# Optimization experiments

Measured on AMD Instinct MI355X. Metric: run time of the kernel, lower is better.

Reference implementation:

```python
import math
import jax, jax.numpy as jnp
import numpy as np

N_HEAD = 32
N_KV_HEADS = 8
HEAD_DIM = 128
N_EMBD = 4096
B, T = 1, 2048


def apply_rope(x, cos, sin):
    # x: [B, H, T, D]; cos/sin: [T, D//2] -> broadcast over B, H
    half = x.shape[-1] // 2
    c = cos[None, None, :, :]
    s = sin[None, None, :, :]
    x1, x2 = x[..., :half], x[..., half:]
    return jnp.concatenate([x1 * c - x2 * s, x2 * c + x1 * s], axis=-1).astype(x.dtype)


def setup_inputs() -> dict:
    key = jax.random.key(0)
    ks = jax.random.split(key, 7)
    x = jax.random.normal(ks[0], (B, T, N_EMBD), dtype=jnp.float32)
    # realistic rope tables
    inv_freq = 1.0 / (10000.0 ** (jnp.arange(0, HEAD_DIM, 2, dtype=jnp.float32) / HEAD_DIM))
    angles = jnp.arange(T, dtype=jnp.float32)[:, None] * inv_freq[None, :]  # [T, D//2]
    rope_cos = jnp.cos(angles)
    rope_sin = jnp.sin(angles)
    sc = 1.0 / math.sqrt(N_EMBD)
    Wq = jax.random.normal(ks[1], (N_EMBD, N_HEAD * HEAD_DIM), dtype=jnp.float32) * sc
    Wk = jax.random.normal(ks[2], (N_EMBD, N_KV_HEADS * HEAD_DIM), dtype=jnp.float32) * sc
    Wv = jax.random.normal(ks[3], (N_EMBD, N_KV_HEADS * HEAD_DIM), dtype=jnp.float32) * sc
    Wo = jax.random.normal(ks[4], (N_HEAD * HEAD_DIM, N_EMBD), dtype=jnp.float32) * sc
    return {"x": x, "rope_cos": rope_cos, "rope_sin": rope_sin,
            "Wq": Wq, "Wk": Wk, "Wv": Wv, "Wo": Wo}


def reference(x, rope_cos, rope_sin, Wq, Wk, Wv, Wo):
    Bx, Tx, _ = x.shape
    n_rep = N_HEAD // N_KV_HEADS
    # QKV projections (no bias, Llama-style) -> [B, H, T, D]
    q = jnp.einsum('btd,df->btf', x, Wq).reshape(Bx, Tx, N_HEAD, HEAD_DIM).transpose(0, 2, 1, 3)
    k = jnp.einsum('btd,df->btf', x, Wk).reshape(Bx, Tx, N_KV_HEADS, HEAD_DIM).transpose(0, 2, 1, 3)
    v = jnp.einsum('btd,df->btf', x, Wv).reshape(Bx, Tx, N_KV_HEADS, HEAD_DIM).transpose(0, 2, 1, 3)
    q = apply_rope(q, rope_cos, rope_sin)
    k = apply_rope(k, rope_cos, rope_sin)
    # GQA: repeat_interleave kv heads to match query heads
    if n_rep > 1:
        k = jnp.repeat(k, n_rep, axis=1)
        v = jnp.repeat(v, n_rep, axis=1)
    scale = 1.0 / math.sqrt(HEAD_DIM)
    scores = jnp.einsum('bhqd,bhkd->bhqk', q, k) * scale  # [B, H, T, T]
    causal = jnp.tril(jnp.ones((Tx, Tx), dtype=bool))
    scores = jnp.where(causal[None, None, :, :], scores, jnp.finfo(scores.dtype).min)
    attn = jax.nn.softmax(scores, axis=-1)
    y = jnp.einsum('bhqk,bhkd->bhqd', attn, v)
    y = y.transpose(0, 2, 1, 3).reshape(Bx, Tx, N_HEAD * HEAD_DIM)
    return jnp.einsum('btf,fd->btd', y, Wo)
```

## Files before the change

kernel.cpp:

```cpp
#include <hip/hip_runtime.h>

typedef unsigned short u16;
typedef __bf16 bf16x8 __attribute__((ext_vector_type(8)));
typedef float f32x4 __attribute__((ext_vector_type(4)));

__device__ __forceinline__ u16 f2bf(float f) {
    unsigned int u = __builtin_bit_cast(unsigned int, f);
    u += 0x7fffu + ((u >> 16) & 1u);
    return (u16)(u >> 16);
}
__device__ __forceinline__ float bf2f(u16 b) {
    unsigned int u = ((unsigned int)b) << 16;
    return __builtin_bit_cast(float, u);
}
__device__ __forceinline__ void load_lds16(const void* g, void* l) {
    __builtin_amdgcn_global_load_lds((__attribute__((address_space(1))) void*)(g),
                                     (__attribute__((address_space(3))) void*)(l), 16, 0, 0);
}
__device__ __forceinline__ f32x4 mfma16(bf16x8 a, bf16x8 b, f32x4 c) {
    return __builtin_amdgcn_mfma_f32_16x16x32_bf16(a, b, c, 0, 0, 0);
}

__global__ __launch_bounds__(256) void k_cvt_bf16(const float* __restrict__ in,
                                                  u16* __restrict__ out, int n4) {
    int i = blockIdx.x * 256 + threadIdx.x;
    if (i < n4) {
        float4 v = ((const float4*)in)[i];
        unsigned int lo = (unsigned int)f2bf(v.x) | ((unsigned int)f2bf(v.y) << 16);
        unsigned int hi = (unsigned int)f2bf(v.z) | ((unsigned int)f2bf(v.w) << 16);
        ((uint2*)out)[i] = make_uint2(lo, hi);
    }
}

__global__ __launch_bounds__(256) void k_transpose_cvt(const float* __restrict__ W,
                                                       u16* __restrict__ Wt, int K, int N) {
    __shared__ u16 t[32][33];
    int tx = threadIdx.x & 31, ty = threadIdx.x >> 5;
    int n0 = blockIdx.x * 32, k0 = blockIdx.y * 32;
#pragma unroll
    for (int i = 0; i < 4; i++)
        t[ty + i * 8][tx] = f2bf(W[(size_t)(k0 + ty + i * 8) * N + n0 + tx]);
    __syncthreads();
#pragma unroll
    for (int i = 0; i < 4; i++)
        Wt[(size_t)(n0 + ty + i * 8) * K + k0 + tx] = t[tx][ty + i * 8];
}

__global__ __launch_bounds__(256) void k_transpose_v(const u16* __restrict__ QKV,
                                                     u16* __restrict__ Vt) {
    __shared__ u16 t[32][33];
    int tx = threadIdx.x & 31, ty = threadIdx.x >> 5;
    int t0 = blockIdx.x * 32, d0 = blockIdx.y * 32, kh = blockIdx.z;
#pragma unroll
    for (int i = 0; i < 4; i++)
        t[ty + i * 8][tx] = QKV[(size_t)(t0 + ty + i * 8) * 6144 + 5120 + kh * 128 + d0 + tx];
    __syncthreads();
#pragma unroll
    for (int i = 0; i < 4; i++)
        Vt[((size_t)kh * 128 + d0 + ty + i * 8) * 2048 + t0 + tx] = t[tx][ty + i * 8];
}

__global__ __launch_bounds__(256) void k_rope2(u16* __restrict__ QKV,
                                               const float* __restrict__ cosT,
                                               const float* __restrict__ sinT) {
    int idx = blockIdx.x * 256 + threadIdx.x;
    int d = idx & 63;
    int h = (idx >> 6) % 40;
    int tp = idx / (40 * 64);
    int col = h < 32 ? h * 128 : 4096 + (h - 32) * 128;
    size_t base = (size_t)tp * 6144 + col + d;
    float q1 = bf2f(QKV[base]), q2 = bf2f(QKV[base + 64]);
    float c = cosT[tp * 64 + d], s = sinT[tp * 64 + d];
    QKV[base] = f2bf(q1 * c - q2 * s);
    QKV[base + 64] = f2bf(q2 * c + q1 * s);
}

template <typename OutT>
__global__ __launch_bounds__(256) void k_gemm_bt(const u16* __restrict__ A,
                                                 const u16* __restrict__ B,
                                                 OutT* __restrict__ C, int M, int N, int K) {
    __shared__ u16 sA[128 * 32];
    __shared__ u16 sB[128 * 32];
    const int tid = threadIdx.x;
    const int wave = tid >> 6, lane = tid & 63;
    const int gx = (int)gridDim.x;
    const int nwg = gx * (int)gridDim.y;
    const int orig = (int)blockIdx.y * gx + (int)blockIdx.x;
    const int qq = nwg >> 3, rr8 = nwg & 7;
    const int xcd = orig & 7, bidx = orig >> 3;
    const int swz = (xcd < rr8 ? xcd * (qq + 1) : rr8 * (qq + 1) + (xcd - rr8) * qq) + bidx;
    const int m0 = (swz / gx) << 7;
    const int n0 = (swz % gx) << 7;
    const int wr = (wave >> 1) << 6, wc = (wave & 1) << 6;
    const int r0 = tid >> 2;
    const int kb = (tid & 3) << 4;
    const int fr = lane & 15;
    const int fkb = (lane >> 4) << 4;

    f32x4 acc[4][4] = {};
    const char* gA = (const char*)A + ((size_t)(m0 + r0) * K) * 2 + kb;
    const char* gB = (const char*)B + ((size_t)(n0 + r0) * K) * 2 + kb;
    char* lA = (char*)sA + wave * 1024;
    char* lB = (char*)sB + wave * 1024;
    const size_t rowskip = (size_t)64 * K * 2;

    for (int k0 = 0; k0 < K; k0 += 32) {
        load_lds16(gA, lA);
        load_lds16(gA + rowskip, lA + 4096);
        load_lds16(gB, lB);
        load_lds16(gB + rowskip, lB + 4096);
        gA += 64; gB += 64;
        __syncthreads();
        bf16x8 af[4], bg[4];
#pragma unroll
        for (int i = 0; i < 4; i++)
            af[i] = *(const bf16x8*)((const char*)sA + ((wr + i * 16 + fr) << 6) + fkb);
#pragma unroll
        for (int j = 0; j < 4; j++)
            bg[j] = *(const bf16x8*)((const char*)sB + ((wc + j * 16 + fr) << 6) + fkb);
#pragma unroll
        for (int i = 0; i < 4; i++)
#pragma unroll
            for (int j = 0; j < 4; j++)
                acc[i][j] = mfma16(af[i], bg[j], acc[i][j]);
        __syncthreads();
    }
    const int rr = (lane >> 4) << 2, cc = lane & 15;
#pragma unroll
    for (int i = 0; i < 4; i++)
#pragma unroll
        for (int j = 0; j < 4; j++)
#pragma unroll
            for (int r = 0; r < 4; r++) {
                float v = acc[i][j][r];
                OutT sv;
                if constexpr (sizeof(OutT) == 2) sv = f2bf(v); else sv = v;
                C[(size_t)(m0 + wr + i * 16 + rr + r) * N + (n0 + wc + j * 16 + cc)] = sv;
            }
}

__global__ __launch_bounds__(256, 2) void k_attn(const u16* __restrict__ Q,
                                                 const u16* __restrict__ K,
                                                 const u16* __restrict__ Vt,
                                                 u16* __restrict__ Y) {
    __shared__ u16 kt[64 * 128];
    __shared__ u16 vt[128 * 64];
    __shared__ u16 pl[4 * 16 * 64];
    const int tid = threadIdx.x;
    const int wave = tid >> 6, lane = tid & 63;
    const int l15 = lane & 15, l4 = lane >> 4;
    const int h = blockIdx.y, kh = h >> 2;
    const float scale = 0.08838834764831845f;

    char* ktb = (char*)kt;
    char* vtb = (char*)vt;
    char* plb = (char*)pl + wave * 2048;

#pragma unroll 1
    for (int qsel = 0; qsel < 2; qsel++) {
        const int qt = qsel == 0 ? blockIdx.x : 31 - blockIdx.x;
        const int qw = qt * 64 + wave * 16;

        bf16x8 aq[4];
#pragma unroll
        for (int kf = 0; kf < 4; kf++)
            aq[kf] = *(const bf16x8*)(Q + (size_t)(qw + l15) * 6144 + h * 128 + kf * 32 + l4 * 8);

        f32x4 o[8] = {};
        float mrow[4], lrow[4];
#pragma unroll
        for (int rg = 0; rg < 4; rg++) { mrow[rg] = -1e30f; lrow[rg] = 0.f; }

        const int nkt = qt + 1;
        for (int it = 0; it < nkt; ++it) {
            const int kbase = it << 6;
#pragma unroll
            for (int p = 0; p < 4; p++) {
                int ol = wave * 4096 + p * 1024 + lane * 16;
                int key = ol >> 8, db = ol & 255;
                int src = db ^ ((key & 7) << 4);
                load_lds16((const char*)K + ((size_t)(kbase + key) * 6144 + kh * 128) * 2 + src,
                           ktb + wave * 4096 + p * 1024);
            }
#pragma unroll
            for (int p = 0; p < 4; p++) {
                int ol = wave * 4096 + p * 1024 + lane * 16;
                int d = ol >> 7, kb2 = ol & 127;
                int src = kb2 ^ ((d & 7) << 4);
                load_lds16((const char*)Vt + ((size_t)(kh * 128 + d) * 2048 + kbase) * 2 + src,
                           vtb + wave * 4096 + p * 1024);
            }
            __syncthreads();

            f32x4 s[4];
#pragma unroll
            for (int tc = 0; tc < 4; tc++) {
                bf16x8 bk[4];
                const int key = tc * 16 + l15;
                const int swz = (key & 7) << 4;
#pragma unroll
                for (int kf = 0; kf < 4; kf++)
                    bk[kf] = *(const bf16x8*)(ktb + key * 256 + ((kf * 64 + l4 * 16) ^ swz));
                f32x4 sv = {0.f, 0.f, 0.f, 0.f};
#pragma unroll
                for (int kf = 0; kf < 4; kf++) sv = mfma16(aq[kf], bk[kf], sv);
                s[tc] = sv;
            }
#pragma unroll
            for (int rg = 0; rg < 4; rg++) {
                const int qrow = qw + l4 * 4 + rg;
                float mx = -1e30f;
#pragma unroll
                for (int tc = 0; tc < 4; tc++) {
                    float v = s[tc][rg] * scale;
                    int key = kbase + tc * 16 + l15;
                    v = (key > qrow) ? -1e30f : v;
                    s[tc][rg] = v;
                    mx = fmaxf(mx, v);
                }
                mx = fmaxf(mx, __shfl_xor(mx, 1));
                mx = fmaxf(mx, __shfl_xor(mx, 2));
                mx = fmaxf(mx, __shfl_xor(mx, 4));
                mx = fmaxf(mx, __shfl_xor(mx, 8));
                const float mold = mrow[rg];
                const float mnew = fmaxf(mold, mx);
                const float corr = __expf(mold - mnew);
                mrow[rg] = mnew;
                float rs = 0.f;
#pragma unroll
                for (int tc = 0; tc < 4; tc++) {
                    float p = __expf(s[tc][rg] - mnew);
                    s[tc][rg] = p;
                    rs += p;
                }
                rs += __shfl_xor(rs, 1);
                rs += __shfl_xor(rs, 2);
                rs += __shfl_xor(rs, 4);
                rs += __shfl_xor(rs, 8);
                lrow[rg] = lrow[rg] * corr + rs;
#pragma unroll
                for (int dc = 0; dc < 8; dc++) o[dc][rg] *= corr;
            }
#pragma unroll
            for (int rg = 0; rg < 4; rg++) {
                const int row = l4 * 4 + rg;
                const int swz = (row & 7) << 4;
#pragma unroll
                for (int tc = 0; tc < 4; tc++) {
                    const int cb = (tc * 16 + l15) * 2;
                    *(u16*)(plb + row * 128 + (cb ^ swz)) = f2bf(s[tc][rg]);
                }
            }
            bf16x8 pa[2];
            {
                const int row = l15;
                const int swz = (row & 7) << 4;
#pragma unroll
                for (int kf = 0; kf < 2; kf++)
                    pa[kf] = *(const bf16x8*)(plb + row * 128 + ((kf * 64 + l4 * 16) ^ swz));
            }
#pragma unroll
            for (int dc = 0; dc < 8; dc++) {
                bf16x8 vf[2];
                const int d = dc * 16 + l15;
                const int swz = (d & 7) << 4;
#pragma unroll
                for (int kf = 0; kf < 2; kf++)
                    vf[kf] = *(const bf16x8*)(vtb + d * 128 + ((kf * 64 + l4 * 16) ^ swz));
                o[dc] = mfma16(pa[0], vf[0], o[dc]);
                o[dc] = mfma16(pa[1], vf[1], o[dc]);
            }
            __syncthreads();
        }
#pragma unroll
        for (int rg = 0; rg < 4; rg++) {
            const float inv = 1.f / lrow[rg];
            const int row = qw + l4 * 4 + rg;
#pragma unroll
            for (int dc = 0; dc < 8; dc++)
                Y[(size_t)row * 4096 + h * 128 + dc * 16 + l15] = f2bf(o[dc][rg] * inv);
        }
        __syncthreads();
    }
}

extern "C" void kernel_launch(void* const* d_in, const int* in_sizes, int n_in,
                              void* d_out, int out_size, void* d_ws, size_t ws_size,
                              hipStream_t stream) {
    const float* x  = (const float*)d_in[0];
    const float* rc = (const float*)d_in[1];
    const float* rs = (const float*)d_in[2];
    const float* Wq = (const float*)d_in[3];
    const float* Wk = (const float*)d_in[4];
    const float* Wv = (const float*)d_in[5];
    const float* Wo = (const float*)d_in[6];
    float* out = (float*)d_out;

    char* ws = (char*)d_ws;
    u16* xb  = (u16*)(ws);
    u16* Wt  = (u16*)(ws + 16777216);
    u16* QKV = (u16*)(ws + 67108864);
    u16* Vtb = (u16*)(ws + 92274688);
    u16* Y   = xb;

    k_cvt_bf16<<<8192, 256, 0, stream>>>(x, xb, 2097152);
    k_transpose_cvt<<<dim3(128, 128), 256, 0, stream>>>(Wq, Wt, 4096, 4096);
    k_transpose_cvt<<<dim3(32, 128), 256, 0, stream>>>(Wk, Wt + (size_t)4096 * 4096, 4096, 1024);
    k_transpose_cvt<<<dim3(32, 128), 256, 0, stream>>>(Wv, Wt + (size_t)5120 * 4096, 4096, 1024);
    k_gemm_bt<u16><<<dim3(48, 16), 256, 0, stream>>>(xb, Wt, QKV, 2048, 6144, 4096);
    k_rope2<<<20480, 256, 0, stream>>>(QKV, rc, rs);
    k_transpose_v<<<dim3(64, 4, 8), 256, 0, stream>>>(QKV, Vtb);
    k_attn<<<dim3(16, 32), 256, 0, stream>>>(QKV, QKV + 4096, Vtb, Y);
    k_transpose_cvt<<<dim3(128, 128), 256, 0, stream>>>(Wo, Wt, 4096, 4096);
    k_gemm_bt<float><<<dim3(32, 16), 256, 0, stream>>>(Y, Wt, out, 2048, 4096, 4096);
}
```

Before: 570.4 us.

## Replace 128x128 GEMM with double-buffered 256x256 tile kernel using 512 threads

Both projection GEMMs now use a new kernel with 256x256 output tiles, 8 waves and 128KB of LDS. Global-to-LDS loads are double-buffered and split into two half-K stages synchronised with vmcnt waits. The LDS layout is swizzled to avoid bank conflicts, and s_setprio is raised around the MFMA bursts. The aim is more operand reuse per load and overlapping loads with compute, at the cost of far fewer workgroups (192 and 128), which leaves some CUs idle. Local variables in the attention kernel are renamed so they do not clash with the new macros.

```diff
diff --git a/kernel.cpp b/kernel.cpp
--- a/kernel.cpp
+++ b/kernel.cpp
@@ -75,67 +75,109 @@
     QKV[base + 64] = f2bf(q2 * c + q1 * s);
 }
 
+
+#define STAGE(G, base0, ldsOff, kt, kh)                                                     \
+    {                                                                                       \
+        _Pragma("unroll") for (int p = 0; p < 2; p++) {                                     \
+            int o = p * 8192 + o0;                                                          \
+            int row = o >> 6;                                                               \
+            int kb = (o & 48) ^ (((row >> 1) & 3) << 4);                                    \
+            load_lds16((const char*)(G) +                                                   \
+                           ((size_t)(base0 + row) * K + (kt) * 64 + (kh) * 32) * 2 + kb,    \
+                       lb + (ldsOff) + p * 8192 + waveB);                                   \
+        }                                                                                   \
+    }
+#define LDA(kh, bufv)                                                                       \
+    _Pragma("unroll") for (int fm = 0; fm < 8; fm++) {                                      \
+        int row = wmBase + fm * 16 + l15;                                                   \
+        af[fm] = *(const bf16x8*)(lb + (bufv) * 32768 + (kh) * 16384 + row * 64 +           \
+                                  ((l4 * 16) ^ (((row >> 1) & 3) << 4)));                   \
+    }
+#define LDB(fn, kh, bufv, dst)                                                              \
+    {                                                                                       \
+        int row = wnBase + (fn) * 16 + l15;                                                 \
+        dst = *(const bf16x8*)(lb + 65536 + (bufv) * 32768 + (kh) * 16384 + row * 64 +      \
+                               ((l4 * 16) ^ (((row >> 1) & 3) << 4)));                      \
+    }
+#define MFMA2(fnA, fnB)                                                                     \
+    __builtin_amdgcn_s_setprio(1);                                                          \
+    _Pragma("unroll") for (int fm = 0; fm < 8; fm++) {                                      \
+        acc[fm][fnA] = mfma16(af[fm], b0, acc[fm][fnA]);                                    \
+        acc[fm][fnB] = mfma16(af[fm], b1, acc[fm][fnB]);                                    \
+    }                                                                                       \
+    __builtin_amdgcn_s_setprio(0);
+
 template <typename OutT>
-__global__ __launch_bounds__(256) void k_gemm_bt(const u16* __restrict__ A,
-                                                 const u16* __restrict__ B,
-                                                 OutT* __restrict__ C, int M, int N, int K) {
-    __shared__ u16 sA[128 * 32];
-    __shared__ u16 sB[128 * 32];
+__global__ __launch_bounds__(512, 2) void k_gemm256(const u16* __restrict__ A,
+                                                    const u16* __restrict__ B,
+                                                    OutT* __restrict__ C, int M, int N, int K) {
+    __shared__ u16 lds[65536];
     const int tid = threadIdx.x;
-    const int wave = tid >> 6, lane = tid & 63;
+    const int lane = tid & 63, l15 = lane & 15, l4 = lane >> 4;
+    const int wave = tid >> 6;
+    const int wmBase = (wave >> 2) << 7;
+    const int wnBase = (wave & 3) << 6;
+    const int waveB = wave << 10;
+    const int o0 = tid * 16;
+
     const int gx = (int)gridDim.x;
     const int nwg = gx * (int)gridDim.y;
     const int orig = (int)blockIdx.y * gx + (int)blockIdx.x;
     const int qq = nwg >> 3, rr8 = nwg & 7;
     const int xcd = orig & 7, bidx = orig >> 3;
     const int swz = (xcd < rr8 ? xcd * (qq + 1) : rr8 * (qq + 1) + (xcd - rr8) * qq) + bidx;
-    const int m0 = (swz / gx) << 7;
-    const int n0 = (swz % gx) << 7;
-    const int wr = (wave >> 1) << 6, wc = (wave & 1) << 6;
-    const int r0 = tid >> 2;
-    const int kb = (tid & 3) << 4;
-    const int fr = lane & 15;
-    const int fkb = (lane >> 4) << 4;
-
-    f32x4 acc[4][4] = {};
-    const char* gA = (const char*)A + ((size_t)(m0 + r0) * K) * 2 + kb;
-    const char* gB = (const char*)B + ((size_t)(n0 + r0) * K) * 2 + kb;
-    char* lA = (char*)sA + wave * 1024;
-    char* lB = (char*)sB + wave * 1024;
-    const size_t rowskip = (size_t)64 * K * 2;
-
-    for (int k0 = 0; k0 < K; k0 += 32) {
-        load_lds16(gA, lA);
-        load_lds16(gA + rowskip, lA + 4096);
-        load_lds16(gB, lB);
-        load_lds16(gB + rowskip, lB + 4096);
-        gA += 64; gB += 64;
-        __syncthreads();
-        bf16x8 af[4], bg[4];
-#pragma unroll
-        for (int i = 0; i < 4; i++)
-            af[i] = *(const bf16x8*)((const char*)sA + ((wr + i * 16 + fr) << 6) + fkb);
-#pragma unroll
-        for (int j = 0; j < 4; j++)
-            bg[j] = *(const bf16x8*)((const char*)sB + ((wc + j * 16 + fr) << 6) + fkb);
-#pragma unroll
-        for (int i = 0; i < 4; i++)
-#pragma unroll
-            for (int j = 0; j < 4; j++)
-                acc[i][j] = mfma16(af[i], bg[j], acc[i][j]);
-        __syncthreads();
-    }
-    const int rr = (lane >> 4) << 2, cc = lane & 15;
-#pragma unroll
-    for (int i = 0; i < 4; i++)
-#pragma unroll
-        for (int j = 0; j < 4; j++)
+    const int m0 = (swz / gx) << 8;
+    const int n0 = (swz % gx) << 8;
+
+    char* lb = (char*)lds;
+    f32x4 acc[8][4] = {};
+    bf16x8 af[8], b0, b1;
+
+    STAGE(A, m0, 0, 0, 0);
+    STAGE(B, n0, 65536, 0, 0);
+    STAGE(A, m0, 16384, 0, 1);
+    STAGE(B, n0, 65536 + 16384, 0, 1);
+
+    const int NT = K >> 6;
+#pragma unroll 1
+    for (int t = 0; t < NT; ++t) {
+        const int buf = t & 1, nbuf = buf ^ 1;
+        const int nt = (t + 1 < NT) ? t + 1 : 0;
+        const int ab = nbuf * 32768, bb = 65536 + nbuf * 32768;
+        asm volatile("s_waitcnt vmcnt(4)" ::: "memory");
+        __builtin_amdgcn_s_barrier();
+        LDA(0, buf);
+        LDB(0, 0, buf, b0);
+        LDB(1, 0, buf, b1);
+        STAGE(A, m0, ab, nt, 0);
+        MFMA2(0, 1);
+        LDB(2, 0, buf, b0);
+        LDB(3, 0, buf, b1);
+        STAGE(B, n0, bb, nt, 0);
+        MFMA2(2, 3);
+        asm volatile("s_waitcnt vmcnt(4)" ::: "memory");
+        __builtin_amdgcn_s_barrier();
+        LDA(1, buf);
+        LDB(0, 1, buf, b0);
+        LDB(1, 1, buf, b1);
+        STAGE(A, m0, ab + 16384, nt, 1);
+        MFMA2(0, 1);
+        LDB(2, 1, buf, b0);
+        LDB(3, 1, buf, b1);
+        STAGE(B, n0, bb + 16384, nt, 1);
+        MFMA2(2, 3);
+    }
+#pragma unroll
+    for (int fm = 0; fm < 8; fm++)
+#pragma unroll
+        for (int fn = 0; fn < 4; fn++)
 #pragma unroll
             for (int r = 0; r < 4; r++) {
-                float v = acc[i][j][r];
+                float v = acc[fm][fn][r];
                 OutT sv;
                 if constexpr (sizeof(OutT) == 2) sv = f2bf(v); else sv = v;
-                C[(size_t)(m0 + wr + i * 16 + rr + r) * N + (n0 + wc + j * 16 + cc)] = sv;
+                C[(size_t)(m0 + wmBase + fm * 16 + l4 * 4 + r) * N +
+                  (n0 + wnBase + fn * 16 + l15)] = sv;
             }
 }
 
@@ -197,10 +239,10 @@
             for (int tc = 0; tc < 4; tc++) {
                 bf16x8 bk[4];
                 const int key = tc * 16 + l15;
-                const int swz = (key & 7) << 4;
+                const int swzk = (key & 7) << 4;
 #pragma unroll
                 for (int kf = 0; kf < 4; kf++)
-                    bk[kf] = *(const bf16x8*)(ktb + key * 256 + ((kf * 64 + l4 * 16) ^ swz));
+                    bk[kf] = *(const bf16x8*)(ktb + key * 256 + ((kf * 64 + l4 * 16) ^ swzk));
                 f32x4 sv = {0.f, 0.f, 0.f, 0.f};
 #pragma unroll
                 for (int kf = 0; kf < 4; kf++) sv = mfma16(aq[kf], bk[kf], sv);
@@ -226,47 +268,47 @@
                 const float mnew = fmaxf(mold, mx);
                 const float corr = __expf(mold - mnew);
                 mrow[rg] = mnew;
-                float rs = 0.f;
+                float rsum = 0.f;
 #pragma unroll
                 for (int tc = 0; tc < 4; tc++) {
                     float p = __expf(s[tc][rg] - mnew);
                     s[tc][rg] = p;
-                    rs += p;
+                    rsum += p;
                 }
-                rs += __shfl_xor(rs, 1);
-                rs += __shfl_xor(rs, 2);
-                rs += __shfl_xor(rs, 4);
-                rs += __shfl_xor(rs, 8);
-                lrow[rg] = lrow[rg] * corr + rs;
+                rsum += __shfl_xor(rsum, 1);
+                rsum += __shfl_xor(rsum, 2);
+                rsum += __shfl_xor(rsum, 4);
+                rsum += __shfl_xor(rsum, 8);
+                lrow[rg] = lrow[rg] * corr + rsum;
 #pragma unroll
                 for (int dc = 0; dc < 8; dc++) o[dc][rg] *= corr;
             }
 #pragma unroll
             for (int rg = 0; rg < 4; rg++) {
                 const int row = l4 * 4 + rg;
-                const int swz = (row & 7) << 4;
+                const int swzp = (row & 7) << 4;
 #pragma unroll
                 for (int tc = 0; tc < 4; tc++) {
                     const int cb = (tc * 16 + l15) * 2;
-                    *(u16*)(plb + row * 128 + (cb ^ swz)) = f2bf(s[tc][rg]);
+                    *(u16*)(plb + row * 128 + (cb ^ swzp)) = f2bf(s[tc][rg]);
                 }
             }
             bf16x8 pa[2];
             {
                 const int row = l15;
-                const int swz = (row & 7) << 4;
+                const int swzp = (row & 7) << 4;
 #pragma unroll
                 for (int kf = 0; kf < 2; kf++)
-                    pa[kf] = *(const bf16x8*)(plb + row * 128 + ((kf * 64 + l4 * 16) ^ swz));
+                    pa[kf] = *(const bf16x8*)(plb + row * 128 + ((kf * 64 + l4 * 16) ^ swzp));
             }
 #pragma unroll
             for (int dc = 0; dc < 8; dc++) {
                 bf16x8 vf[2];
                 const int d = dc * 16 + l15;
-                const int swz = (d & 7) << 4;
+                const int swzv = (d & 7) << 4;
 #pragma unroll
                 for (int kf = 0; kf < 2; kf++)
-                    vf[kf] = *(const bf16x8*)(vtb + d * 128 + ((kf * 64 + l4 * 16) ^ swz));
+                    vf[kf] = *(const bf16x8*)(vtb + d * 128 + ((kf * 64 + l4 * 16) ^ swzv));
                 o[dc] = mfma16(pa[0], vf[0], o[dc]);
                 o[dc] = mfma16(pa[1], vf[1], o[dc]);
             }
@@ -307,10 +349,10 @@
     k_transpose_cvt<<<dim3(128, 128), 256, 0, stream>>>(Wq, Wt, 4096, 4096);
     k_transpose_cvt<<<dim3(32, 128), 256, 0, stream>>>(Wk, Wt + (size_t)4096 * 4096, 4096, 1024);
     k_transpose_cvt<<<dim3(32, 128), 256, 0, stream>>>(Wv, Wt + (size_t)5120 * 4096, 4096, 1024);
-    k_gemm_bt<u16><<<dim3(48, 16), 256, 0, stream>>>(xb, Wt, QKV, 2048, 6144, 4096);
+    k_gemm256<u16><<<dim3(24, 8), 512, 0, stream>>>(xb, Wt, QKV, 2048, 6144, 4096);
     k_rope2<<<20480, 256, 0, stream>>>(QKV, rc, rs);
     k_transpose_v<<<dim3(64, 4, 8), 256, 0, stream>>>(QKV, Vtb);
     k_attn<<<dim3(16, 32), 256, 0, stream>>>(QKV, QKV + 4096, Vtb, Y);
     k_transpose_cvt<<<dim3(128, 128), 256, 0, stream>>>(Wo, Wt, 4096, 4096);
-    k_gemm_bt<float><<<dim3(32, 16), 256, 0, stream>>>(Y, Wt, out, 2048, 4096, 4096);
-}
+    k_gemm256<float><<<dim3(16, 8), 512, 0, stream>>>(Y, Wt, out, 2048, 4096, 4096);
+}
```

New measurement: 528.0 us. 1.08x faster.
